# Kernel optimization log

Hardware: AMD Instinct MI355X
Metric: run time of the kernel (lower is better)

Reference implementation:

```python
import jax, jax.numpy as jnp
import numpy as np

INPUT_SIZE = 14
HIDDEN = 128
BATCH = 2048
SEQ = 512


def setup_inputs() -> dict:
    key = jax.random.key(0)
    ks = jax.random.split(key, 11)
    s_in = 1.0 / np.sqrt(HIDDEN)  # PyTorch LSTM init: U(-1/sqrt(H), 1/sqrt(H))
    def u(k, shape):
        return jax.random.uniform(k, shape, jnp.float32, -s_in, s_in)
    return {
        "x": jax.random.normal(ks[0], (BATCH, SEQ, INPUT_SIZE), jnp.float32),
        # layer 0 (input_size -> hidden), gate order i,f,g,o as in PyTorch
        "Wih0": u(ks[1], (4 * HIDDEN, INPUT_SIZE)),
        "Whh0": u(ks[2], (4 * HIDDEN, HIDDEN)),
        "bih0": u(ks[3], (4 * HIDDEN,)),
        "bhh0": u(ks[4], (4 * HIDDEN,)),
        # layer 1 (hidden -> hidden)
        "Wih1": u(ks[5], (4 * HIDDEN, HIDDEN)),
        "Whh1": u(ks[6], (4 * HIDDEN, HIDDEN)),
        "bih1": u(ks[7], (4 * HIDDEN,)),
        "bhh1": u(ks[8], (4 * HIDDEN,)),
        # final linear hidden -> 1
        "Wfc": u(ks[9], (1, HIDDEN)),
        "bfc": u(ks[10], (1,)),
    }


def _lstm_layer(x, Wih, Whh, bih, bhh):
    """Single LSTM layer over (B, T, I). Returns (ys (B,T,H), h_final (B,H))."""
    B, T, _ = x.shape
    H = Whh.shape[1]
    # precompute input projections for all timesteps: (B, T, 4H)
    xp = jnp.einsum('bti,gi->btg', x, Wih) + (bih + bhh)
    xp = jnp.swapaxes(xp, 0, 1)  # (T, B, 4H) for scan

    def step(carry, xt):
        h, c = carry
        gates = xt + h @ Whh.T  # (B, 4H)
        i, f, g, o = jnp.split(gates, 4, axis=-1)
        i = jax.nn.sigmoid(i)
        f = jax.nn.sigmoid(f)
        g = jnp.tanh(g)
        o = jax.nn.sigmoid(o)
        c = f * c + i * g
        h = o * jnp.tanh(c)
        return (h, c), h

    h0 = jnp.zeros((B, H), x.dtype)
    c0 = jnp.zeros((B, H), x.dtype)
    (hT, _), ys = jax.lax.scan(step, (h0, c0), xp)
    return jnp.swapaxes(ys, 0, 1), hT


def reference(x, Wih0, Whh0, bih0, bhh0, Wih1, Whh1, bih1, bhh1, Wfc, bfc):
    # dropout is inference no-op (model baseline assumes eval mode)
    y0, _ = _lstm_layer(x, Wih0, Whh0, bih0, bhh0)
    _, h_last = _lstm_layer(y0, Wih1, Whh1, bih1, bhh1)
    out = h_last @ Wfc.T + bfc  # (B, 1)
    return jax.nn.sigmoid(out)
```

## Files before the change

kernel.cpp:

```cpp
#include <hip/hip_runtime.h>
#include <hip/hip_bf16.h>

#define HID 128
#define SEQ 512
#define INS 14
#define BC 16
#define X0STRIDE 40
#define X1STRIDE 264
#define NFRAG0 10240
#define NFRAG1 16384
#define W1BASE (NFRAG0 * 8)

typedef __attribute__((ext_vector_type(8))) short bs8;
typedef __attribute__((ext_vector_type(4))) float f4;

__device__ __forceinline__ short f2bf(float f) {
    union { float f; unsigned u; } a; a.f = f;
    unsigned u = a.u;
    u += 0x7fffu + ((u >> 16) & 1u);
    return (short)(u >> 16);
}
__device__ __forceinline__ float bf2f(short s) {
    union { unsigned u; float f; } a;
    a.u = ((unsigned)(unsigned short)s) << 16;
    return a.f;
}
__device__ __forceinline__ float sigm(float x) {
    return __builtin_amdgcn_rcpf(1.f + __builtin_amdgcn_exp2f(x * -1.44269504f));
}

__global__ void lstm_prep(
    const float* __restrict__ Wih0, const float* __restrict__ Whh0,
    const float* __restrict__ bih0, const float* __restrict__ bhh0,
    const float* __restrict__ Wih1, const float* __restrict__ Whh1,
    short* __restrict__ wsw)
{
    int f = blockIdx.x * 256 + threadIdx.x;
    if (f >= NFRAG0 + NFRAG1) return;
    if (f < NFRAG0) {
        int lane = f & 63, t = f >> 6;
        int ks = t % 5, gw = t / 5, g = gw & 3, wv = gw >> 2;
        int row = g * HID + wv * 16 + (lane & 15);
        int kbase = ks * 32 + (lane >> 4) * 8;
        for (int j = 0; j < 8; ++j) {
            int k = kbase + j;
            float v;
            if (k < INS)        v = Wih0[row * INS + k];
            else if (k == INS)  v = bih0[row] + bhh0[row];
            else if (k < 32)    v = 0.f;
            else                v = Whh0[row * HID + (k - 32)];
            wsw[f * 8 + j] = f2bf(v);
        }
    } else {
        int fl = f - NFRAG0;
        int lane = fl & 63, t = fl >> 6;
        int ks = t & 7, g = (t >> 3) & 3, wv = t >> 5;
        int row = g * HID + wv * 16 + (lane & 15);
        int kbase = ks * 32 + (lane >> 4) * 8;
        for (int j = 0; j < 8; ++j) {
            int k = kbase + j;
            float v = (k < HID) ? Wih1[row * HID + k] : Whh1[row * HID + (k - HID)];
            wsw[f * 8 + j] = f2bf(v);
        }
    }
}

__global__ __attribute__((amdgpu_flat_work_group_size(512, 512)))
__attribute__((amdgpu_waves_per_eu(2, 2))) void lstm_fused(
    const float* __restrict__ x,
    const float* __restrict__ Wfc,  const float* __restrict__ bfc,
    const float* __restrict__ bih1, const float* __restrict__ bhh1,
    const short* __restrict__ wsw,
    float* __restrict__ out)
{
    __shared__ __align__(16) short xh0[2][BC][X0STRIDE];
    __shared__ __align__(16) short xh1[2][BC][X1STRIDE];
    __shared__ __align__(16) short wlds[8][4][4][64][8];

    const int tid  = threadIdx.x;
    const int lane = tid & 63;
    const int wv   = tid >> 6;
    const int col  = lane & 15;
    const int quad = lane >> 4;
    const int u    = wv * 16 + col;
    const int b0   = blockIdx.x * BC;

    const short* wb0 = wsw + ((wv * 20) * 64 + lane) * 8;
    const short* wb1 = wsw + W1BASE + ((wv * 32) * 64 + lane) * 8;
#define DW0(g,ks) const bs8 w0_##g##_##ks = *(const bs8*)(wb0 + ((g)*5+(ks))*512);
#define DW1(g,ks) const bs8 w1_##g##_##ks = *(const bs8*)(wb1 + ((g)*8+(ks))*512);
    DW0(0,0) DW0(0,1) DW0(0,2) DW0(0,3) DW0(0,4)
    DW0(1,0) DW0(1,1) DW0(1,2) DW0(1,3) DW0(1,4)
    DW0(2,0) DW0(2,1) DW0(2,2) DW0(2,3) DW0(2,4)
    DW0(3,0) DW0(3,1) DW0(3,2) DW0(3,3) DW0(3,4)
    DW1(0,0) DW1(0,1) DW1(0,2) DW1(0,3)
    DW1(1,0) DW1(1,1) DW1(1,2) DW1(1,3)
    DW1(2,0) DW1(2,1) DW1(2,2) DW1(2,3)
    DW1(3,0) DW1(3,1) DW1(3,2) DW1(3,3)

    const float b1_0 = bih1[0 * HID + u] + bhh1[0 * HID + u];
    const float b1_1 = bih1[1 * HID + u] + bhh1[1 * HID + u];
    const float b1_2 = bih1[2 * HID + u] + bhh1[2 * HID + u];
    const float b1_3 = bih1[3 * HID + u] + bhh1[3 * HID + u];

    for (int idx = tid; idx < 2 * BC * X0STRIDE; idx += 512) ((short*)xh0)[idx] = 0;
    for (int idx = tid; idx < 2 * BC * X1STRIDE; idx += 512) ((short*)xh1)[idx] = 0;
#pragma unroll
    for (int f = 0; f < 16; ++f) {
        int ksm4 = f >> 2, g = f & 3;
        *(bs8*)&wlds[wv][ksm4][g][lane][0] =
            *(const bs8*)(wsw + W1BASE +
                (((wv * 4 + g) * 8 + (ksm4 + 4)) * 64 + lane) * 8);
    }
    __syncthreads();
    if (tid < 2 * BC) xh0[tid >> 4][tid & 15][INS] = (short)0x3f80;

    const int  xm = wv * 2 + (lane >> 5);
    const int  xi = lane & 31;
    const bool xldr = (xi < INS);
    const float* xp = xldr ? (x + ((size_t)(b0 + xm) * SEQ) * INS + xi) : x;
    float xv = xldr ? xp[0] : 0.f;

    float c0_0 = 0.f, c0_1 = 0.f, c0_2 = 0.f, c0_3 = 0.f;
    float c1_0 = 0.f, c1_1 = 0.f, c1_2 = 0.f, c1_3 = 0.f;
    const int aoff = quad * 8;

#define L1KR(ks, AF) { \
        acc1_0 = __builtin_amdgcn_mfma_f32_16x16x32_bf16(AF, w1_0_##ks, acc1_0, 0,0,0); \
        acc1_1 = __builtin_amdgcn_mfma_f32_16x16x32_bf16(AF, w1_1_##ks, acc1_1, 0,0,0); \
        acc1_2 = __builtin_amdgcn_mfma_f32_16x16x32_bf16(AF, w1_2_##ks, acc1_2, 0,0,0); \
        acc1_3 = __builtin_amdgcn_mfma_f32_16x16x32_bf16(AF, w1_3_##ks, acc1_3, 0,0,0); }
#define L1KL(ks, AF) { \
        const bs8 u0 = *(const bs8*)&wlds[wv][(ks)-4][0][lane][0]; \
        const bs8 u1 = *(const bs8*)&wlds[wv][(ks)-4][1][lane][0]; \
        const bs8 u2 = *(const bs8*)&wlds[wv][(ks)-4][2][lane][0]; \
        const bs8 u3 = *(const bs8*)&wlds[wv][(ks)-4][3][lane][0]; \
        acc1_0 = __builtin_amdgcn_mfma_f32_16x16x32_bf16(AF, u0, acc1_0, 0,0,0); \
        acc1_1 = __builtin_amdgcn_mfma_f32_16x16x32_bf16(AF, u1, acc1_1, 0,0,0); \
        acc1_2 = __builtin_amdgcn_mfma_f32_16x16x32_bf16(AF, u2, acc1_2, 0,0,0); \
        acc1_3 = __builtin_amdgcn_mfma_f32_16x16x32_bf16(AF, u3, acc1_3, 0,0,0); }
#define L0K(ks, AF) { \
        acc0_0 = __builtin_amdgcn_mfma_f32_16x16x32_bf16(AF, w0_0_##ks, acc0_0, 0,0,0); \
        acc0_1 = __builtin_amdgcn_mfma_f32_16x16x32_bf16(AF, w0_1_##ks, acc0_1, 0,0,0); \
        acc0_2 = __builtin_amdgcn_mfma_f32_16x16x32_bf16(AF, w0_2_##ks, acc0_2, 0,0,0); \
        acc0_3 = __builtin_amdgcn_mfma_f32_16x16x32_bf16(AF, w0_3_##ks, acc0_3, 0,0,0); }

#define CELLH(A0, A1, A2, A3, cvar, r, HOUT) { \
        float ei = __builtin_amdgcn_exp2f(A0[r] * -1.44269504f); \
        float ef = __builtin_amdgcn_exp2f(A1[r] * -1.44269504f); \
        float eg = __builtin_amdgcn_exp2f(A2[r] * -2.88539008f); \
        float eo = __builtin_amdgcn_exp2f(A3[r] * -1.44269504f); \
        float Di = 1.f + ei, Df = 1.f + ef, Dg = 1.f + eg, Do = 1.f + eo; \
        float rP = __builtin_amdgcn_rcpf(Df * Di * Dg); \
        float num = __builtin_fmaf(cvar * Di, Dg, (1.f - eg) * Df); \
        cvar = num * rP; \
        float ec = __builtin_amdgcn_exp2f(cvar * -2.88539008f); \
        float rQ = __builtin_amdgcn_rcpf((1.f + ec) * Do); \
        HOUT = (1.f - ec) * rQ; }

#define STOREPAIR(HA, HB, J, ROW, COLOFF) { \
        unsigned pk; \
        asm("v_cvt_pk_bf16_f32 %0, %1, %2" : "=v"(pk) : "v"(HA), "v"(HB)); \
        xh1[ROW][quad * 4 + 2*(J)][(COLOFF) + u]     = (short)pk; \
        xh1[ROW][quad * 4 + 2*(J) + 1][(COLOFF) + u] = (short)(pk >> 16); }

#define CELL4_0(ROW) { \
        float h0_, h1_, h2_, h3_; \
        CELLH(acc0_0, acc0_1, acc0_2, acc0_3, c0_0, 0, h0_) \
        CELLH(acc0_0, acc0_1, acc0_2, acc0_3, c0_1, 1, h1_) \
        CELLH(acc0_0, acc0_1, acc0_2, acc0_3, c0_2, 2, h2_) \
        CELLH(acc0_0, acc0_1, acc0_2, acc0_3, c0_3, 3, h3_) \
        STOREPAIR(h0_, h1_, 0, ROW, 0) STOREPAIR(h2_, h3_, 1, ROW, 0) }

#define CELL1H(r, HOUT) CELLH(acc1_0, acc1_1, acc1_2, acc1_3, c1_##r, r, HOUT)

    {
        const int p = 0, q = 1;
        if (xldr) xh0[p][xm][xi] = f2bf(xv);
        float xnext = xldr ? xp[INS] : 0.f;
        __syncthreads();
        const bs8 afx = *(const bs8*)&xh0[p][col][aoff];
        const bs8 af0 = *(const bs8*)&xh1[p][col][0 * 32 + aoff];
        const bs8 af1 = *(const bs8*)&xh1[p][col][1 * 32 + aoff];
        const bs8 af2 = *(const bs8*)&xh1[p][col][2 * 32 + aoff];
        const bs8 af3 = *(const bs8*)&xh1[p][col][3 * 32 + aoff];
        f4 acc0_0 = {0.f,0.f,0.f,0.f}, acc0_1 = {0.f,0.f,0.f,0.f};
        f4 acc0_2 = {0.f,0.f,0.f,0.f}, acc0_3 = {0.f,0.f,0.f,0.f};
        L0K(0, afx) L0K(1, af0) L0K(2, af1) L0K(3, af2) L0K(4, af3)
        CELL4_0(q)
        xv = xnext;
    }

    for (int t = 1; t < SEQ; ++t) {
        const int p = t & 1, q = p ^ 1;
        if (xldr) xh0[p][xm][xi] = f2bf(xv);
        float xnext = (xldr && (t + 1 < SEQ)) ? xp[(t + 1) * INS] : 0.f;
        __syncthreads();

        const bs8 afx = *(const bs8*)&xh0[p][col][aoff];
        const bs8 af0 = *(const bs8*)&xh1[p][col][0 * 32 + aoff];
        const bs8 af1 = *(const bs8*)&xh1[p][col][1 * 32 + aoff];
        const bs8 af2 = *(const bs8*)&xh1[p][col][2 * 32 + aoff];
        const bs8 af3 = *(const bs8*)&xh1[p][col][3 * 32 + aoff];
        const bs8 af4 = *(const bs8*)&xh1[p][col][4 * 32 + aoff];
        const bs8 af5 = *(const bs8*)&xh1[p][col][5 * 32 + aoff];
        const bs8 af6 = *(const bs8*)&xh1[p][col][6 * 32 + aoff];
        const bs8 af7 = *(const bs8*)&xh1[p][col][7 * 32 + aoff];

        f4 acc1_0 = {b1_0, b1_0, b1_0, b1_0};
        f4 acc1_1 = {b1_1, b1_1, b1_1, b1_1};
        f4 acc1_2 = {b1_2, b1_2, b1_2, b1_2};
        f4 acc1_3 = {b1_3, b1_3, b1_3, b1_3};
        L1KR(0, af0) L1KR(1, af1) L1KR(2, af2) L1KR(3, af3)
        L1KL(4, af4) L1KL(5, af5) L1KL(6, af6) L1KL(7, af7)

        f4 acc0_0 = {0.f,0.f,0.f,0.f}, acc0_1 = {0.f,0.f,0.f,0.f};
        f4 acc0_2 = {0.f,0.f,0.f,0.f}, acc0_3 = {0.f,0.f,0.f,0.f};
        float g0_, g1_, g2_, g3_;
        L0K(0, afx) CELL1H(0, g0_)
        L0K(1, af0) CELL1H(1, g1_)
        L0K(2, af1) CELL1H(2, g2_)
        L0K(3, af2) CELL1H(3, g3_)
        L0K(4, af3)
        STOREPAIR(g0_, g1_, 0, q, HID) STOREPAIR(g2_, g3_, 1, q, HID)
        CELL4_0(q)

        xv = xnext;
    }

    {
        const int p = 0, q = 1;
        __syncthreads();
        const bs8 af0 = *(const bs8*)&xh1[p][col][0 * 32 + aoff];
        const bs8 af1 = *(const bs8*)&xh1[p][col][1 * 32 + aoff];
        const bs8 af2 = *(const bs8*)&xh1[p][col][2 * 32 + aoff];
        const bs8 af3 = *(const bs8*)&xh1[p][col][3 * 32 + aoff];
        const bs8 af4 = *(const bs8*)&xh1[p][col][4 * 32 + aoff];
        const bs8 af5 = *(const bs8*)&xh1[p][col][5 * 32 + aoff];
        const bs8 af6 = *(const bs8*)&xh1[p][col][6 * 32 + aoff];
        const bs8 af7 = *(const bs8*)&xh1[p][col][7 * 32 + aoff];
        f4 acc1_0 = {b1_0, b1_0, b1_0, b1_0};
        f4 acc1_1 = {b1_1, b1_1, b1_1, b1_1};
        f4 acc1_2 = {b1_2, b1_2, b1_2, b1_2};
        f4 acc1_3 = {b1_3, b1_3, b1_3, b1_3};
        L1KR(0, af0) L1KR(1, af1) L1KR(2, af2) L1KR(3, af3)
        L1KL(4, af4) L1KL(5, af5) L1KL(6, af6) L1KL(7, af7)
        float g0_, g1_, g2_, g3_;
        CELL1H(0, g0_) CELL1H(1, g1_) CELL1H(2, g2_) CELL1H(3, g3_)
        STOREPAIR(g0_, g1_, 0, q, HID) STOREPAIR(g2_, g3_, 1, q, HID)
    }
    __syncthreads();

    if (tid < BC) {
        float s = bfc[0];
#pragma unroll 8
        for (int k2 = 0; k2 < HID; ++k2)
            s += bf2f(xh1[1][tid][HID + k2]) * Wfc[k2];
        out[b0 + tid] = sigm(s);
    }
}

extern "C" void kernel_launch(void* const* d_in, const int* in_sizes, int n_in,
                              void* d_out, int out_size, void* d_ws, size_t ws_size,
                              hipStream_t stream) {
    const float* x    = (const float*)d_in[0];
    const float* Wih0 = (const float*)d_in[1];
    const float* Whh0 = (const float*)d_in[2];
    const float* bih0 = (const float*)d_in[3];
    const float* bhh0 = (const float*)d_in[4];
    const float* Wih1 = (const float*)d_in[5];
    const float* Whh1 = (const float*)d_in[6];
    const float* bih1 = (const float*)d_in[7];
    const float* bhh1 = (const float*)d_in[8];
    const float* Wfc  = (const float*)d_in[9];
    const float* bfc  = (const float*)d_in[10];
    float* out = (float*)d_out;
    short* wsw = (short*)d_ws;

    int nfrag = NFRAG0 + NFRAG1;
    lstm_prep<<<(nfrag + 255) / 256, 256, 0, stream>>>(Wih0, Whh0, bih0, bhh0,
                                                       Wih1, Whh1, wsw);
    dim3 grid(2048 / BC);
    dim3 block(512);
    lstm_fused<<<grid, block, 0, stream>>>(x, Wfc, bfc, bih1, bhh1, wsw, out);
}
```

Measured before the change: 961.2 us.

## Swizzle hidden-state LDS layout and keep more layer-1 weight fragments in registers

Applies an XOR swizzle to the column index of the shared hidden-state buffer, on both the bf16 stores and the MFMA A-fragment loads, to cut LDS bank conflicts. It also moves one more k-slice of layer-1 weights from LDS into registers (5 register-resident slices, 3 in LDS), which shrinks the LDS weight buffer and the per-step LDS reads. The cost is higher VGPR pressure under the fixed waves-per-eu limit, which could cause spills.

```diff
diff --git a/kernel.cpp b/kernel.cpp
--- a/kernel.cpp
+++ b/kernel.cpp
@@ -75,7 +75,7 @@
 {
     __shared__ __align__(16) short xh0[2][BC][X0STRIDE];
     __shared__ __align__(16) short xh1[2][BC][X1STRIDE];
-    __shared__ __align__(16) short wlds[8][4][4][64][8];
+    __shared__ __align__(16) short wlds[8][3][4][64][8];
 
     const int tid  = threadIdx.x;
     const int lane = tid & 63;
@@ -84,6 +84,8 @@
     const int quad = lane >> 4;
     const int u    = wv * 16 + col;
     const int b0   = blockIdx.x * BC;
+    const int skey = (quad & 2) << 3;
+    const int rkey = (col  & 8) << 1;
 
     const short* wb0 = wsw + ((wv * 20) * 64 + lane) * 8;
     const short* wb1 = wsw + W1BASE + ((wv * 32) * 64 + lane) * 8;
@@ -93,10 +95,10 @@
     DW0(1,0) DW0(1,1) DW0(1,2) DW0(1,3) DW0(1,4)
     DW0(2,0) DW0(2,1) DW0(2,2) DW0(2,3) DW0(2,4)
     DW0(3,0) DW0(3,1) DW0(3,2) DW0(3,3) DW0(3,4)
-    DW1(0,0) DW1(0,1) DW1(0,2) DW1(0,3)
-    DW1(1,0) DW1(1,1) DW1(1,2) DW1(1,3)
-    DW1(2,0) DW1(2,1) DW1(2,2) DW1(2,3)
-    DW1(3,0) DW1(3,1) DW1(3,2) DW1(3,3)
+    DW1(0,0) DW1(0,1) DW1(0,2) DW1(0,3) DW1(0,4)
+    DW1(1,0) DW1(1,1) DW1(1,2) DW1(1,3) DW1(1,4)
+    DW1(2,0) DW1(2,1) DW1(2,2) DW1(2,3) DW1(2,4)
+    DW1(3,0) DW1(3,1) DW1(3,2) DW1(3,3) DW1(3,4)
 
     const float b1_0 = bih1[0 * HID + u] + bhh1[0 * HID + u];
     const float b1_1 = bih1[1 * HID + u] + bhh1[1 * HID + u];
@@ -106,11 +108,11 @@
     for (int idx = tid; idx < 2 * BC * X0STRIDE; idx += 512) ((short*)xh0)[idx] = 0;
     for (int idx = tid; idx < 2 * BC * X1STRIDE; idx += 512) ((short*)xh1)[idx] = 0;
 #pragma unroll
-    for (int f = 0; f < 16; ++f) {
-        int ksm4 = f >> 2, g = f & 3;
-        *(bs8*)&wlds[wv][ksm4][g][lane][0] =
+    for (int f = 0; f < 12; ++f) {
+        int m = f >> 2, g = f & 3;
+        *(bs8*)&wlds[wv][m][g][lane][0] =
             *(const bs8*)(wsw + W1BASE +
-                (((wv * 4 + g) * 8 + (ksm4 + 4)) * 64 + lane) * 8);
+                (((wv * 4 + g) * 8 + (m + 5)) * 64 + lane) * 8);
     }
     __syncthreads();
     if (tid < 2 * BC) xh0[tid >> 4][tid & 15][INS] = (short)0x3f80;
@@ -131,10 +133,10 @@
         acc1_2 = __builtin_amdgcn_mfma_f32_16x16x32_bf16(AF, w1_2_##ks, acc1_2, 0,0,0); \
         acc1_3 = __builtin_amdgcn_mfma_f32_16x16x32_bf16(AF, w1_3_##ks, acc1_3, 0,0,0); }
 #define L1KL(ks, AF) { \
-        const bs8 u0 = *(const bs8*)&wlds[wv][(ks)-4][0][lane][0]; \
-        const bs8 u1 = *(const bs8*)&wlds[wv][(ks)-4][1][lane][0]; \
-        const bs8 u2 = *(const bs8*)&wlds[wv][(ks)-4][2][lane][0]; \
-        const bs8 u3 = *(const bs8*)&wlds[wv][(ks)-4][3][lane][0]; \
+        const bs8 u0 = *(const bs8*)&wlds[wv][(ks)-5][0][lane][0]; \
+        const bs8 u1 = *(const bs8*)&wlds[wv][(ks)-5][1][lane][0]; \
+        const bs8 u2 = *(const bs8*)&wlds[wv][(ks)-5][2][lane][0]; \
+        const bs8 u3 = *(const bs8*)&wlds[wv][(ks)-5][3][lane][0]; \
         acc1_0 = __builtin_amdgcn_mfma_f32_16x16x32_bf16(AF, u0, acc1_0, 0,0,0); \
         acc1_1 = __builtin_amdgcn_mfma_f32_16x16x32_bf16(AF, u1, acc1_1, 0,0,0); \
         acc1_2 = __builtin_amdgcn_mfma_f32_16x16x32_bf16(AF, u2, acc1_2, 0,0,0); \
@@ -144,6 +146,8 @@
         acc0_1 = __builtin_amdgcn_mfma_f32_16x16x32_bf16(AF, w0_1_##ks, acc0_1, 0,0,0); \
         acc0_2 = __builtin_amdgcn_mfma_f32_16x16x32_bf16(AF, w0_2_##ks, acc0_2, 0,0,0); \
         acc0_3 = __builtin_amdgcn_mfma_f32_16x16x32_bf16(AF, w0_3_##ks, acc0_3, 0,0,0); }
+
+#define AFR(P, ks) (*(const bs8*)&xh1[P][col][((ks) * 32 + aoff) ^ rkey])
 
 #define CELLH(A0, A1, A2, A3, cvar, r, HOUT) { \
         float ei = __builtin_amdgcn_exp2f(A0[r] * -1.44269504f); \
@@ -161,8 +165,8 @@
 #define STOREPAIR(HA, HB, J, ROW, COLOFF) { \
         unsigned pk; \
         asm("v_cvt_pk_bf16_f32 %0, %1, %2" : "=v"(pk) : "v"(HA), "v"(HB)); \
-        xh1[ROW][quad * 4 + 2*(J)][(COLOFF) + u]     = (short)pk; \
-        xh1[ROW][quad * 4 + 2*(J) + 1][(COLOFF) + u] = (short)(pk >> 16); }
+        xh1[ROW][quad * 4 + 2*(J)][(COLOFF) + (u ^ skey)]     = (short)pk; \
+        xh1[ROW][quad * 4 + 2*(J) + 1][(COLOFF) + (u ^ skey)] = (short)(pk >> 16); }
 
 #define CELL4_0(ROW) { \
         float h0_, h1_, h2_, h3_; \
@@ -180,10 +184,10 @@
         float xnext = xldr ? xp[INS] : 0.f;
         __syncthreads();
         const bs8 afx = *(const bs8*)&xh0[p][col][aoff];
-        const bs8 af0 = *(const bs8*)&xh1[p][col][0 * 32 + aoff];
-        const bs8 af1 = *(const bs8*)&xh1[p][col][1 * 32 + aoff];
-        const bs8 af2 = *(const bs8*)&xh1[p][col][2 * 32 + aoff];
-        const bs8 af3 = *(const bs8*)&xh1[p][col][3 * 32 + aoff];
+        const bs8 af0 = AFR(p, 0);
+        const bs8 af1 = AFR(p, 1);
+        const bs8 af2 = AFR(p, 2);
+        const bs8 af3 = AFR(p, 3);
         f4 acc0_0 = {0.f,0.f,0.f,0.f}, acc0_1 = {0.f,0.f,0.f,0.f};
         f4 acc0_2 = {0.f,0.f,0.f,0.f}, acc0_3 = {0.f,0.f,0.f,0.f};
         L0K(0, afx) L0K(1, af0) L0K(2, af1) L0K(3, af2) L0K(4, af3)
@@ -198,21 +202,21 @@
         __syncthreads();
 
         const bs8 afx = *(const bs8*)&xh0[p][col][aoff];
-        const bs8 af0 = *(const bs8*)&xh1[p][col][0 * 32 + aoff];
-        const bs8 af1 = *(const bs8*)&xh1[p][col][1 * 32 + aoff];
-        const bs8 af2 = *(const bs8*)&xh1[p][col][2 * 32 + aoff];
-        const bs8 af3 = *(const bs8*)&xh1[p][col][3 * 32 + aoff];
-        const bs8 af4 = *(const bs8*)&xh1[p][col][4 * 32 + aoff];
-        const bs8 af5 = *(const bs8*)&xh1[p][col][5 * 32 + aoff];
-        const bs8 af6 = *(const bs8*)&xh1[p][col][6 * 32 + aoff];
-        const bs8 af7 = *(const bs8*)&xh1[p][col][7 * 32 + aoff];
+        const bs8 af0 = AFR(p, 0);
+        const bs8 af1 = AFR(p, 1);
+        const bs8 af2 = AFR(p, 2);
+        const bs8 af3 = AFR(p, 3);
+        const bs8 af4 = AFR(p, 4);
+        const bs8 af5 = AFR(p, 5);
+        const bs8 af6 = AFR(p, 6);
+        const bs8 af7 = AFR(p, 7);
 
         f4 acc1_0 = {b1_0, b1_0, b1_0, b1_0};
         f4 acc1_1 = {b1_1, b1_1, b1_1, b1_1};
         f4 acc1_2 = {b1_2, b1_2, b1_2, b1_2};
         f4 acc1_3 = {b1_3, b1_3, b1_3, b1_3};
-        L1KR(0, af0) L1KR(1, af1) L1KR(2, af2) L1KR(3, af3)
-        L1KL(4, af4) L1KL(5, af5) L1KL(6, af6) L1KL(7, af7)
+        L1KR(0, af0) L1KR(1, af1) L1KR(2, af2) L1KR(3, af3) L1KR(4, af4)
+        L1KL(5, af5) L1KL(6, af6) L1KL(7, af7)
 
         f4 acc0_0 = {0.f,0.f,0.f,0.f}, acc0_1 = {0.f,0.f,0.f,0.f};
         f4 acc0_2 = {0.f,0.f,0.f,0.f}, acc0_3 = {0.f,0.f,0.f,0.f};
@@ -231,20 +235,20 @@
     {
         const int p = 0, q = 1;
         __syncthreads();
-        const bs8 af0 = *(const bs8*)&xh1[p][col][0 * 32 + aoff];
-        const bs8 af1 = *(const bs8*)&xh1[p][col][1 * 32 + aoff];
-        const bs8 af2 = *(const bs8*)&xh1[p][col][2 * 32 + aoff];
-        const bs8 af3 = *(const bs8*)&xh1[p][col][3 * 32 + aoff];
-        const bs8 af4 = *(const bs8*)&xh1[p][col][4 * 32 + aoff];
-        const bs8 af5 = *(const bs8*)&xh1[p][col][5 * 32 + aoff];
-        const bs8 af6 = *(const bs8*)&xh1[p][col][6 * 32 + aoff];
-        const bs8 af7 = *(const bs8*)&xh1[p][col][7 * 32 + aoff];
+        const bs8 af0 = AFR(p, 0);
+        const bs8 af1 = AFR(p, 1);
+        const bs8 af2 = AFR(p, 2);
+        const bs8 af3 = AFR(p, 3);
+        const bs8 af4 = AFR(p, 4);
+        const bs8 af5 = AFR(p, 5);
+        const bs8 af6 = AFR(p, 6);
+        const bs8 af7 = AFR(p, 7);
         f4 acc1_0 = {b1_0, b1_0, b1_0, b1_0};
         f4 acc1_1 = {b1_1, b1_1, b1_1, b1_1};
         f4 acc1_2 = {b1_2, b1_2, b1_2, b1_2};
         f4 acc1_3 = {b1_3, b1_3, b1_3, b1_3};
-        L1KR(0, af0) L1KR(1, af1) L1KR(2, af2) L1KR(3, af3)
-        L1KL(4, af4) L1KL(5, af5) L1KL(6, af6) L1KL(7, af7)
+        L1KR(0, af0) L1KR(1, af1) L1KR(2, af2) L1KR(3, af3) L1KR(4, af4)
+        L1KL(5, af5) L1KL(6, af6) L1KL(7, af7)
         float g0_, g1_, g2_, g3_;
         CELL1H(0, g0_) CELL1H(1, g1_) CELL1H(2, g2_) CELL1H(3, g3_)
         STOREPAIR(g0_, g1_, 0, q, HID) STOREPAIR(g2_, g3_, 1, q, HID)
@@ -252,10 +256,11 @@
     __syncthreads();
 
     if (tid < BC) {
+        const int key_fc = (tid & 8) << 1;
         float s = bfc[0];
 #pragma unroll 8
         for (int k2 = 0; k2 < HID; ++k2)
-            s += bf2f(xh1[1][tid][HID + k2]) * Wfc[k2];
+            s += bf2f(xh1[1][tid][HID + (k2 ^ key_fc)]) * Wfc[k2];
         out[b0 + tid] = sigm(s);
     }
 }
```

Measured after the change: 990.0 us. 1.03x slower.
